# Kernel optimization log

Measured on AMD Instinct MI355X. Metric: run time of the kernel, lower is better.

## Reference

```python
import jax, jax.numpy as jnp
import numpy as np

N, D, H, G = 262144, 256, 8, 2048
DH = D // H  # 32


def setup_inputs() -> dict:
    key = jax.random.key(0)
    ks = jax.random.split(key, 12)
    s = 0.02
    x = jax.random.normal(ks[0], (N, D), jnp.float32)
    # equal-size sets: batch[i] = set id, ptr = CSR boundaries (consistent pair)
    batch = jnp.repeat(jnp.arange(G, dtype=jnp.int64), N // G)
    ptr = jnp.arange(G + 1, dtype=jnp.int64) * (N // G)
    rn = lambda k, sh: jax.random.normal(k, sh, jnp.float32) * s
    return {
        "x": x, "ptr": ptr, "batch": batch,
        "lin_w": rn(ks[1], (D, D)), "lin_b": jnp.zeros((D,), jnp.float32),
        "seed": rn(ks[2], (D,)),
        "wq": rn(ks[3], (D, D)), "bq": jnp.zeros((D,), jnp.float32),
        "wk": rn(ks[4], (D, D)), "bk": jnp.zeros((D,), jnp.float32),
        "wv": rn(ks[5], (D, D)), "bv": jnp.zeros((D,), jnp.float32),
        "wo": rn(ks[6], (D, D)), "bo": jnp.zeros((D,), jnp.float32),
        "mlp_w1": rn(ks[7], (D, D)), "mlp_b1": jnp.zeros((D,), jnp.float32),
        "mlp_w2": rn(ks[8], (D, D)), "mlp_b2": jnp.zeros((D,), jnp.float32),
    }


def gelu(v):
    return jax.nn.gelu(v, approximate=False)  # torch nn.GELU default (erf)


def reference(x, ptr, batch, lin_w, lin_b, seed, wq, bq, wk, bk, wv, bv,
              wo, bo, mlp_w1, mlp_b1, mlp_w2, mlp_b2):
    # pre-projection + GELU
    h = gelu(x @ lin_w + lin_b)                         # [N, D]
    # PMA-style multihead attention pooling over ragged sets
    q = (seed @ wq + bq).reshape(H, DH)                 # learnable seed query per head
    k = (h @ wk + bk).reshape(-1, H, DH)                # [N, H, DH]
    v = (h @ wv + bv).reshape(-1, H, DH)                # [N, H, DH]
    scores = jnp.einsum('nhd,hd->nh', k, q) / jnp.sqrt(jnp.float32(DH))  # [N, H]
    # segment (per-set) numerically-stable softmax
    m = jax.ops.segment_max(scores, batch, num_segments=G)   # [G, H]
    e = jnp.exp(scores - m[batch])
    z = jax.ops.segment_sum(e, batch, num_segments=G)        # [G, H]
    w = e / z[batch]                                         # [N, H] attention weights
    pooled = jax.ops.segment_sum(w[:, :, None] * v, batch, num_segments=G)  # [G, H, DH]
    pooled = pooled.reshape(G, D) @ wo + bo                  # output projection [G, D]
    # 2-layer MLP head (plain_last: no act on final layer; dropout=0 at eval)
    out = gelu(pooled @ mlp_w1 + mlp_b1) @ mlp_w2 + mlp_b2   # [G, D]
    return out
```

## Files before the change

### kernel.cpp

```cpp
#include <hip/hip_runtime.h>
#include <hip/hip_bf16.h>

#define DD 256
#define SETSZ 128
#define NSETS 2048

typedef __attribute__((ext_vector_type(8))) __bf16 bf16x8;
typedef __attribute__((ext_vector_type(8))) unsigned short u16x8;
typedef __attribute__((ext_vector_type(4))) float f32x4;

static __device__ __forceinline__ unsigned short f2bf(float f) {
    unsigned u = __builtin_bit_cast(unsigned, f);
    u += 0x7fffu + ((u >> 16) & 1u);
    return (unsigned short)(u >> 16);
}

static __device__ __forceinline__ float gelu_f(float v) {
    float ax = fabsf(v) * 0.70710678118654752f;
    float t = __builtin_amdgcn_rcpf(__builtin_fmaf(0.3275911f, ax, 1.0f));
    float p = __builtin_fmaf(1.061405429f, t, -1.453152027f);
    p = __builtin_fmaf(p, t, 1.421413741f);
    p = __builtin_fmaf(p, t, -0.284496736f);
    p = __builtin_fmaf(p, t, 0.254829592f);
    p = p * t;
    float er = __builtin_fmaf(-p, __expf(-ax * ax), 1.0f);
    er = copysignf(er, v);
    return 0.5f * v * (1.0f + er);
}

static __device__ __forceinline__ int swz(int row, int cg) {
    return cg ^ (row & 7) ^ ((row >> 3) & 3);
}

#define LGKM_BARRIER() do { \
    asm volatile("s_waitcnt lgkmcnt(0)" ::: "memory"); \
    __builtin_amdgcn_s_barrier(); \
} while (0)

__global__ void prep1_kernel(const float* __restrict__ seed, const float* __restrict__ wq,
                             const float* __restrict__ bq, float* __restrict__ q) {
    int j = threadIdx.x;
    float s = bq[j];
#pragma unroll 16
    for (int d = 0; d < DD; ++d) s += seed[d] * wq[d * DD + j];
    q[j] = s;
}

__global__ void prep2_kernel(const float* __restrict__ lin_w, const float* __restrict__ wv,
                             const float* __restrict__ wk, const float* __restrict__ q,
                             unsigned short* __restrict__ linT, unsigned short* __restrict__ wvT,
                             unsigned short* __restrict__ wkqB) {
    int b = blockIdx.x, t = threadIdx.x;
    if (b < DD) {
        linT[b * DD + t] = f2bf(lin_w[t * DD + b]);
        wvT[b * DD + t]  = f2bf(wv[t * DD + b]);
    } else {
        const float inv = 0.17677669529663687f;
        for (int c = 0; c < 8; ++c) {
            float s = 0.f;
#pragma unroll 8
            for (int j = 0; j < 32; ++j) s += wk[t * DD + c * 32 + j] * q[c * 32 + j];
            wkqB[c * DD + t] = f2bf(s * inv);
        }
        for (int c = 8; c < 16; ++c) wkqB[c * DD + t] = 0;
    }
}

__global__ __launch_bounds__(512, 4)
void attn_pool_kernel(const float* __restrict__ x, const float* __restrict__ lin_b,
                      const float* __restrict__ bv,
                      const unsigned short* __restrict__ linT,
                      const unsigned short* __restrict__ wvT,
                      const unsigned short* __restrict__ wkqB,
                      float* __restrict__ pooled) {
    __shared__ unsigned short xs[SETSZ * DD];
    __shared__ float wbuf[SETSZ][8];
    __shared__ float mzbuf[2][16];
    __shared__ float zbuf[2][16];
    __shared__ float pbuf[2][DD];

    const int g = blockIdx.x;
    const int t = threadIdx.x;
    const int lane = t & 63;
    const int wid = t >> 6;
    const int rh = wid >> 2;
    const int cq = wid & 3;
    const int l15 = lane & 15;
    const int kg = lane >> 4;
    const int colq = cq * 64;
    const int rowbase = rh * 64;
    const long r0 = (long)g * SETSZ;

    {
        const float* bx = x + r0 * DD;
#pragma unroll
        for (int half = 0; half < 2; ++half) {
            float4 L[8];
#pragma unroll
            for (int qq = 0; qq < 4; ++qq) {
                int c = (half * 4 + qq) * 512 + t;
                const float4* src = reinterpret_cast<const float4*>(bx + (c >> 5) * DD + (c & 31) * 8);
                L[2 * qq] = src[0];
                L[2 * qq + 1] = src[1];
            }
#pragma unroll
            for (int qq = 0; qq < 4; ++qq) {
                int c = (half * 4 + qq) * 512 + t;
                int row = c >> 5, cg = c & 31;
                u16x8 v;
                v[0] = f2bf(L[2*qq].x);   v[1] = f2bf(L[2*qq].y);
                v[2] = f2bf(L[2*qq].z);   v[3] = f2bf(L[2*qq].w);
                v[4] = f2bf(L[2*qq+1].x); v[5] = f2bf(L[2*qq+1].y);
                v[6] = f2bf(L[2*qq+1].z); v[7] = f2bf(L[2*qq+1].w);
                *reinterpret_cast<u16x8*>(&xs[row * DD + swz(row, cg) * 8]) = v;
            }
        }
    }
    LGKM_BARRIER();

    f32x4 acc[4][4];
#pragma unroll
    for (int ab = 0; ab < 4; ++ab)
#pragma unroll
        for (int nb = 0; nb < 4; ++nb) acc[ab][nb] = 0.f;

#pragma unroll
    for (int ks = 0; ks < 8; ++ks) {
        bf16x8 A[4], B[4];
#pragma unroll
        for (int ab = 0; ab < 4; ++ab)
            A[ab] = *reinterpret_cast<const bf16x8*>(linT + (colq + 16 * ab + l15) * DD + ks * 32 + kg * 8);
#pragma unroll
        for (int nb = 0; nb < 4; ++nb) {
            int row = rowbase + 16 * nb + l15;
            B[nb] = *reinterpret_cast<const bf16x8*>(&xs[row * DD + swz(row, ks * 4 + kg) * 8]);
        }
#pragma unroll
        for (int ab = 0; ab < 4; ++ab)
#pragma unroll
            for (int nb = 0; nb < 4; ++nb)
                acc[ab][nb] = __builtin_amdgcn_mfma_f32_16x16x32_bf16(A[ab], B[nb], acc[ab][nb], 0, 0, 0);
    }
    LGKM_BARRIER();

    {
#pragma unroll
        for (int ab = 0; ab < 4; ++ab) {
            const float4 lb4 = *reinterpret_cast<const float4*>(lin_b + colq + 16 * ab + 4 * kg);
            int cg = (colq >> 3) + 2 * ab + (kg >> 1);
#pragma unroll
            for (int nb = 0; nb < 4; ++nb) {
                int row = rowbase + 16 * nb + l15;
                float g0 = gelu_f(acc[ab][nb][0] + lb4.x);
                float g1 = gelu_f(acc[ab][nb][1] + lb4.y);
                float g2 = gelu_f(acc[ab][nb][2] + lb4.z);
                float g3 = gelu_f(acc[ab][nb][3] + lb4.w);
                unsigned d0 = (unsigned)f2bf(g0) | ((unsigned)f2bf(g1) << 16);
                unsigned d1 = (unsigned)f2bf(g2) | ((unsigned)f2bf(g3) << 16);
                *reinterpret_cast<uint2*>(&xs[row * DD + swz(row, cg) * 8 + (kg & 1) * 4]) =
                    make_uint2(d0, d1);
            }
        }
    }
    LGKM_BARRIER();

    f32x4 sacc[4];
    sacc[0] = 0.f; sacc[1] = 0.f; sacc[2] = 0.f; sacc[3] = 0.f;
    if (cq == 0) {
#pragma unroll
        for (int ks = 0; ks < 8; ++ks) {
            bf16x8 Aq = *reinterpret_cast<const bf16x8*>(wkqB + l15 * DD + ks * 32 + kg * 8);
#pragma unroll
            for (int nb = 0; nb < 4; ++nb) {
                int row = rowbase + 16 * nb + l15;
                bf16x8 B = *reinterpret_cast<const bf16x8*>(&xs[row * DD + swz(row, ks * 4 + kg) * 8]);
                sacc[nb] = __builtin_amdgcn_mfma_f32_16x16x32_bf16(Aq, B, sacc[nb], 0, 0, 0);
            }
        }
        float mj[4];
#pragma unroll
        for (int j = 0; j < 4; ++j)
            mj[j] = fmaxf(fmaxf(sacc[0][j], sacc[1][j]), fmaxf(sacc[2][j], sacc[3][j]));
#pragma unroll
        for (int st = 1; st < 16; st <<= 1)
#pragma unroll
            for (int j = 0; j < 4; ++j) mj[j] = fmaxf(mj[j], __shfl_xor(mj[j], st, 64));
        if (l15 == 0) {
            f32x4 mv; mv[0] = mj[0]; mv[1] = mj[1]; mv[2] = mj[2]; mv[3] = mj[3];
            *reinterpret_cast<f32x4*>(&mzbuf[rh][4 * kg]) = mv;
        }
    }
    LGKM_BARRIER();

    if (cq == 0) {
        f32x4 m0 = *reinterpret_cast<const f32x4*>(&mzbuf[0][4 * kg]);
        f32x4 m1 = *reinterpret_cast<const f32x4*>(&mzbuf[1][4 * kg]);
        float mf[4], zj[4];
#pragma unroll
        for (int j = 0; j < 4; ++j) { mf[j] = fmaxf(m0[j], m1[j]); zj[j] = 0.f; }
        f32x4 e4[4];
#pragma unroll
        for (int nb = 0; nb < 4; ++nb)
#pragma unroll
            for (int j = 0; j < 4; ++j) {
                float e = __expf(sacc[nb][j] - mf[j]);
                e4[nb][j] = e;
                zj[j] += e;
            }
#pragma unroll
        for (int st = 1; st < 16; st <<= 1)
#pragma unroll
            for (int j = 0; j < 4; ++j) zj[j] += __shfl_xor(zj[j], st, 64);
        if (l15 == 0) {
            f32x4 zv; zv[0] = zj[0]; zv[1] = zj[1]; zv[2] = zj[2]; zv[3] = zj[3];
            *reinterpret_cast<f32x4*>(&zbuf[rh][4 * kg]) = zv;
        }
        if (kg < 2) {
#pragma unroll
            for (int nb = 0; nb < 4; ++nb) {
                int row = rowbase + 16 * nb + l15;
                *reinterpret_cast<f32x4*>(&wbuf[row][4 * kg]) = e4[nb];
            }
        }
    }
    LGKM_BARRIER();

    f32x4 vacc[4][4];
#pragma unroll
    for (int ab = 0; ab < 4; ++ab)
#pragma unroll
        for (int nb = 0; nb < 4; ++nb) vacc[ab][nb] = 0.f;
#pragma unroll
    for (int ks = 0; ks < 8; ++ks) {
        bf16x8 A[4], B[4];
#pragma unroll
        for (int ab = 0; ab < 4; ++ab)
            A[ab] = *reinterpret_cast<const bf16x8*>(wvT + (colq + 16 * ab + l15) * DD + ks * 32 + kg * 8);
#pragma unroll
        for (int nb = 0; nb < 4; ++nb) {
            int row = rowbase + 16 * nb + l15;
            B[nb] = *reinterpret_cast<const bf16x8*>(&xs[row * DD + swz(row, ks * 4 + kg) * 8]);
        }
#pragma unroll
        for (int ab = 0; ab < 4; ++ab)
#pragma unroll
            for (int nb = 0; nb < 4; ++nb)
                vacc[ab][nb] = __builtin_amdgcn_mfma_f32_16x16x32_bf16(A[ab], B[nb], vacc[ab][nb], 0, 0, 0);
    }

    {
        float w0[4], w1[4];
#pragma unroll
        for (int nb = 0; nb < 4; ++nb) {
            int row = rowbase + 16 * nb + l15;
            w0[nb] = wbuf[row][2 * cq];
            w1[nb] = wbuf[row][2 * cq + 1];
        }
        float v16[16];
#pragma unroll
        for (int ab = 0; ab < 4; ++ab)
#pragma unroll
            for (int j = 0; j < 4; ++j) {
                float s = 0.f;
#pragma unroll
                for (int nb = 0; nb < 4; ++nb)
                    s += (ab < 2 ? w0[nb] : w1[nb]) * vacc[ab][nb][j];
                v16[ab * 4 + j] = s;
            }
        float v8[8], v4[4], v2[2], vf;
        {
            bool b = (l15 & 1);
#pragma unroll
            for (int i = 0; i < 8; ++i) {
                float keep = b ? v16[2 * i + 1] : v16[2 * i];
                float send = b ? v16[2 * i] : v16[2 * i + 1];
                v8[i] = keep + __shfl_xor(send, 1, 64);
            }
        }
        {
            bool b = (l15 >> 1) & 1;
#pragma unroll
            for (int i = 0; i < 4; ++i) {
                float keep = b ? v8[2 * i + 1] : v8[2 * i];
                float send = b ? v8[2 * i] : v8[2 * i + 1];
                v4[i] = keep + __shfl_xor(send, 2, 64);
            }
        }
        {
            bool b = (l15 >> 2) & 1;
#pragma unroll
            for (int i = 0; i < 2; ++i) {
                float keep = b ? v4[2 * i + 1] : v4[2 * i];
                float send = b ? v4[2 * i] : v4[2 * i + 1];
                v2[i] = keep + __shfl_xor(send, 4, 64);
            }
        }
        {
            bool b = (l15 >> 3) & 1;
            float keep = b ? v2[1] : v2[0];
            float send = b ? v2[0] : v2[1];
            vf = keep + __shfl_xor(send, 8, 64);
        }
        int vcol = colq + 16 * (l15 >> 2) + 4 * kg + (l15 & 3);
        pbuf[rh][vcol] = vf;
    }
    LGKM_BARRIER();

    if (t < DD) {
        int hh = t >> 5;
        float z = zbuf[0][hh] + zbuf[1][hh];
        pooled[(long)g * DD + t] = (pbuf[0][t] + pbuf[1][t]) / z + bv[t];
    }
}

__global__ __launch_bounds__(256)
void mlp_kernel(const float* __restrict__ pooled,
                const float* __restrict__ wo, const float* __restrict__ bo,
                const float* __restrict__ w1, const float* __restrict__ b1,
                const float* __restrict__ w2, const float* __restrict__ b2,
                float* __restrict__ out) {
    __shared__ float sa[8][DD];
    __shared__ float sb[8][DD];
    const int c = threadIdx.x;
    const long base = (long)blockIdx.x * 8 * DD;
#pragma unroll
    for (int r = 0; r < 8; ++r) sa[r][c] = pooled[base + r * DD + c];
    __syncthreads();
    {
        float acc[8];
        float bb = bo[c];
#pragma unroll
        for (int r = 0; r < 8; ++r) acc[r] = bb;
#pragma unroll 4
        for (int k = 0; k < DD; ++k) {
            float wvv = wo[k * DD + c];
#pragma unroll
            for (int r = 0; r < 8; ++r) acc[r] += sa[r][k] * wvv;
        }
#pragma unroll
        for (int r = 0; r < 8; ++r) sb[r][c] = acc[r];
    }
    __syncthreads();
    {
        float acc[8];
        float bb = b1[c];
#pragma unroll
        for (int r = 0; r < 8; ++r) acc[r] = bb;
#pragma unroll 4
        for (int k = 0; k < DD; ++k) {
            float wvv = w1[k * DD + c];
#pragma unroll
            for (int r = 0; r < 8; ++r) acc[r] += sb[r][k] * wvv;
        }
#pragma unroll
        for (int r = 0; r < 8; ++r) sa[r][c] = gelu_f(acc[r]);
    }
    __syncthreads();
    {
        float acc[8];
        float bb = b2[c];
#pragma unroll
        for (int r = 0; r < 8; ++r) acc[r] = bb;
#pragma unroll 4
        for (int k = 0; k < DD; ++k) {
            float wvv = w2[k * DD + c];
#pragma unroll
            for (int r = 0; r < 8; ++r) acc[r] += sa[r][k] * wvv;
        }
#pragma unroll
        for (int r = 0; r < 8; ++r) out[base + r * DD + c] = acc[r];
    }
}

extern "C" void kernel_launch(void* const* d_in, const int* in_sizes, int n_in,
                              void* d_out, int out_size, void* d_ws, size_t ws_size,
                              hipStream_t stream) {
    const float* x     = (const float*)d_in[0];
    const float* lin_w = (const float*)d_in[3];
    const float* lin_b = (const float*)d_in[4];
    const float* seed  = (const float*)d_in[5];
    const float* wq    = (const float*)d_in[6];
    const float* bq    = (const float*)d_in[7];
    const float* wk    = (const float*)d_in[8];
    const float* wvp   = (const float*)d_in[10];
    const float* bv    = (const float*)d_in[11];
    const float* wo    = (const float*)d_in[12];
    const float* bo    = (const float*)d_in[13];
    const float* w1    = (const float*)d_in[14];
    const float* b1    = (const float*)d_in[15];
    const float* w2    = (const float*)d_in[16];
    const float* b2    = (const float*)d_in[17];
    float* out = (float*)d_out;

    char* ws = (char*)d_ws;
    float* q             = (float*)ws;
    unsigned short* wkqB = (unsigned short*)(ws + 4096);
    unsigned short* linT = (unsigned short*)(ws + 16384);
    unsigned short* wvT  = (unsigned short*)(ws + 16384 + 131072);
    float* pooled        = (float*)(ws + 16384 + 262144);

    prep1_kernel<<<1, 256, 0, stream>>>(seed, wq, bq, q);
    prep2_kernel<<<257, 256, 0, stream>>>(lin_w, wvp, wk, q, linT, wvT, wkqB);
    attn_pool_kernel<<<NSETS, 512, 0, stream>>>(x, lin_b, bv, linT, wvT, wkqB, pooled);
    mlp_kernel<<<NSETS / 8, 256, 0, stream>>>(pooled, wo, bo, w1, b1, w2, b2, out);
}
```

Baseline: 311.1 us.

## Make attention-pool kernel persistent with double-buffered prefetch of next set

The attention-pool kernel now launches 256 persistent blocks, each looping over 8 sets. It prefetches the next set's fp32 rows into registers while the current set is computed, then converts them into a second LDS buffer. This is meant to hide global load latency behind MFMA work. The cost is double LDS use (128KB), which caps occupancy at one block per CU and raises register pressure from the 16 prefetched float4s. The weight transpose is also rewritten as a 64x64 LDS tiled transpose, and the MLP kernel now handles 4 rows per block instead of 8, giving it more blocks.

```diff
diff --git a/kernel.cpp b/kernel.cpp
--- a/kernel.cpp
+++ b/kernel.cpp
@@ -4,6 +4,8 @@
 #define DD 256
 #define SETSZ 128
 #define NSETS 2048
+#define NBLK 256
+#define SPB (NSETS / NBLK)
 
 typedef __attribute__((ext_vector_type(8))) __bf16 bf16x8;
 typedef __attribute__((ext_vector_type(8))) unsigned short u16x8;
@@ -46,14 +48,31 @@
     q[j] = s;
 }
 
-__global__ void prep2_kernel(const float* __restrict__ lin_w, const float* __restrict__ wv,
-                             const float* __restrict__ wk, const float* __restrict__ q,
-                             unsigned short* __restrict__ linT, unsigned short* __restrict__ wvT,
-                             unsigned short* __restrict__ wkqB) {
+__global__ __launch_bounds__(256)
+void prep2_kernel(const float* __restrict__ lin_w, const float* __restrict__ wv,
+                  const float* __restrict__ wk, const float* __restrict__ q,
+                  unsigned short* __restrict__ linT, unsigned short* __restrict__ wvT,
+                  unsigned short* __restrict__ wkqB) {
+    __shared__ unsigned short tl[64][65];
     int b = blockIdx.x, t = threadIdx.x;
-    if (b < DD) {
-        linT[b * DD + t] = f2bf(lin_w[t * DD + b]);
-        wvT[b * DD + t]  = f2bf(wv[t * DD + b]);
+    if (b < 32) {
+        const float* src = (b & 1) ? wv : lin_w;
+        unsigned short* dst = (b & 1) ? wvT : linT;
+        int tile = b >> 1;
+        int r0 = (tile >> 2) * 64, c0 = (tile & 3) * 64;
+#pragma unroll
+        for (int i = 0; i < 16; ++i) {
+            int idx = i * 256 + t;
+            int r = idx >> 6, c = idx & 63;
+            tl[r][c] = f2bf(src[(r0 + r) * DD + c0 + c]);
+        }
+        __syncthreads();
+#pragma unroll
+        for (int i = 0; i < 16; ++i) {
+            int idx = i * 256 + t;
+            int cc = idx >> 6, rr = idx & 63;
+            dst[(c0 + cc) * DD + r0 + rr] = tl[rr][cc];
+        }
     } else {
         const float inv = 0.17677669529663687f;
         for (int c = 0; c < 8; ++c) {
@@ -66,20 +85,19 @@
     }
 }
 
-__global__ __launch_bounds__(512, 4)
+__global__ __launch_bounds__(512, 1)
 void attn_pool_kernel(const float* __restrict__ x, const float* __restrict__ lin_b,
                       const float* __restrict__ bv,
                       const unsigned short* __restrict__ linT,
                       const unsigned short* __restrict__ wvT,
                       const unsigned short* __restrict__ wkqB,
                       float* __restrict__ pooled) {
-    __shared__ unsigned short xs[SETSZ * DD];
+    __shared__ unsigned short bufs[2][SETSZ * DD];
     __shared__ float wbuf[SETSZ][8];
     __shared__ float mzbuf[2][16];
     __shared__ float zbuf[2][16];
     __shared__ float pbuf[2][DD];
 
-    const int g = blockIdx.x;
     const int t = threadIdx.x;
     const int lane = t & 63;
     const int wid = t >> 6;
@@ -89,61 +107,68 @@
     const int kg = lane >> 4;
     const int colq = cq * 64;
     const int rowbase = rh * 64;
-    const long r0 = (long)g * SETSZ;
+    const long set0 = (long)blockIdx.x * SPB;
 
     {
-        const float* bx = x + r0 * DD;
-#pragma unroll
-        for (int half = 0; half < 2; ++half) {
-            float4 L[8];
-#pragma unroll
-            for (int qq = 0; qq < 4; ++qq) {
-                int c = (half * 4 + qq) * 512 + t;
-                const float4* src = reinterpret_cast<const float4*>(bx + (c >> 5) * DD + (c & 31) * 8);
-                L[2 * qq] = src[0];
-                L[2 * qq + 1] = src[1];
-            }
-#pragma unroll
-            for (int qq = 0; qq < 4; ++qq) {
-                int c = (half * 4 + qq) * 512 + t;
-                int row = c >> 5, cg = c & 31;
-                u16x8 v;
-                v[0] = f2bf(L[2*qq].x);   v[1] = f2bf(L[2*qq].y);
-                v[2] = f2bf(L[2*qq].z);   v[3] = f2bf(L[2*qq].w);
-                v[4] = f2bf(L[2*qq+1].x); v[5] = f2bf(L[2*qq+1].y);
-                v[6] = f2bf(L[2*qq+1].z); v[7] = f2bf(L[2*qq+1].w);
-                *reinterpret_cast<u16x8*>(&xs[row * DD + swz(row, cg) * 8]) = v;
-            }
+        const float* nb = x + set0 * SETSZ * DD;
+#pragma unroll
+        for (int i = 0; i < 8; ++i) {
+            int p = i * 512 + t;
+            float4 a = *reinterpret_cast<const float4*>(nb + p * 8);
+            float4 b = *reinterpret_cast<const float4*>(nb + p * 8 + 4);
+            int row = p >> 5, cg = p & 31;
+            u16x8 v;
+            v[0] = f2bf(a.x); v[1] = f2bf(a.y); v[2] = f2bf(a.z); v[3] = f2bf(a.w);
+            v[4] = f2bf(b.x); v[5] = f2bf(b.y); v[6] = f2bf(b.z); v[7] = f2bf(b.w);
+            *reinterpret_cast<u16x8*>(&bufs[0][row * DD + swz(row, cg) * 8]) = v;
         }
     }
     LGKM_BARRIER();
 
-    f32x4 acc[4][4];
-#pragma unroll
-    for (int ab = 0; ab < 4; ++ab)
-#pragma unroll
-        for (int nb = 0; nb < 4; ++nb) acc[ab][nb] = 0.f;
-
-#pragma unroll
-    for (int ks = 0; ks < 8; ++ks) {
-        bf16x8 A[4], B[4];
+    int cur = 0;
+    for (int s = 0; s < SPB; ++s) {
+        const unsigned short* xs = bufs[cur];
+        unsigned short* xsm = bufs[cur];
+        unsigned short* xn = bufs[cur ^ 1];
+        const bool pf_on = (s + 1 < SPB);
+
+        float4 pf[16];
+        if (pf_on) {
+            const float* nb = x + (set0 + s + 1) * SETSZ * DD;
+#pragma unroll
+            for (int i = 0; i < 8; ++i) {
+                int p = i * 512 + t;
+                pf[2 * i]     = *reinterpret_cast<const float4*>(nb + p * 8);
+                pf[2 * i + 1] = *reinterpret_cast<const float4*>(nb + p * 8 + 4);
+            }
+        }
+        __builtin_amdgcn_sched_barrier(0);
+
+        f32x4 acc[4][4];
 #pragma unroll
         for (int ab = 0; ab < 4; ++ab)
-            A[ab] = *reinterpret_cast<const bf16x8*>(linT + (colq + 16 * ab + l15) * DD + ks * 32 + kg * 8);
-#pragma unroll
-        for (int nb = 0; nb < 4; ++nb) {
-            int row = rowbase + 16 * nb + l15;
-            B[nb] = *reinterpret_cast<const bf16x8*>(&xs[row * DD + swz(row, ks * 4 + kg) * 8]);
-        }
-#pragma unroll
-        for (int ab = 0; ab < 4; ++ab)
-#pragma unroll
-            for (int nb = 0; nb < 4; ++nb)
-                acc[ab][nb] = __builtin_amdgcn_mfma_f32_16x16x32_bf16(A[ab], B[nb], acc[ab][nb], 0, 0, 0);
-    }
-    LGKM_BARRIER();
-
-    {
+#pragma unroll
+            for (int nb = 0; nb < 4; ++nb) acc[ab][nb] = 0.f;
+
+#pragma unroll
+        for (int ks = 0; ks < 8; ++ks) {
+            bf16x8 A[4], B[4];
+#pragma unroll
+            for (int ab = 0; ab < 4; ++ab)
+                A[ab] = *reinterpret_cast<const bf16x8*>(linT + (colq + 16 * ab + l15) * DD + ks * 32 + kg * 8);
+#pragma unroll
+            for (int nb = 0; nb < 4; ++nb) {
+                int row = rowbase + 16 * nb + l15;
+                B[nb] = *reinterpret_cast<const bf16x8*>(&xs[row * DD + swz(row, ks * 4 + kg) * 8]);
+            }
+#pragma unroll
+            for (int ab = 0; ab < 4; ++ab)
+#pragma unroll
+                for (int nb = 0; nb < 4; ++nb)
+                    acc[ab][nb] = __builtin_amdgcn_mfma_f32_16x16x32_bf16(A[ab], B[nb], acc[ab][nb], 0, 0, 0);
+        }
+        LGKM_BARRIER();
+
 #pragma unroll
         for (int ab = 0; ab < 4; ++ab) {
             const float4 lb4 = *reinterpret_cast<const float4*>(lin_b + colq + 16 * ab + 4 * kg);
@@ -157,159 +182,174 @@
                 float g3 = gelu_f(acc[ab][nb][3] + lb4.w);
                 unsigned d0 = (unsigned)f2bf(g0) | ((unsigned)f2bf(g1) << 16);
                 unsigned d1 = (unsigned)f2bf(g2) | ((unsigned)f2bf(g3) << 16);
-                *reinterpret_cast<uint2*>(&xs[row * DD + swz(row, cg) * 8 + (kg & 1) * 4]) =
+                *reinterpret_cast<uint2*>(&xsm[row * DD + swz(row, cg) * 8 + (kg & 1) * 4]) =
                     make_uint2(d0, d1);
             }
         }
-    }
-    LGKM_BARRIER();
-
-    f32x4 sacc[4];
-    sacc[0] = 0.f; sacc[1] = 0.f; sacc[2] = 0.f; sacc[3] = 0.f;
-    if (cq == 0) {
+        LGKM_BARRIER();
+
+        f32x4 sacc[4];
+        sacc[0] = 0.f; sacc[1] = 0.f; sacc[2] = 0.f; sacc[3] = 0.f;
+        if (cq == 0) {
+#pragma unroll
+            for (int ks = 0; ks < 8; ++ks) {
+                bf16x8 Aq = *reinterpret_cast<const bf16x8*>(wkqB + l15 * DD + ks * 32 + kg * 8);
+#pragma unroll
+                for (int nb = 0; nb < 4; ++nb) {
+                    int row = rowbase + 16 * nb + l15;
+                    bf16x8 B = *reinterpret_cast<const bf16x8*>(&xs[row * DD + swz(row, ks * 4 + kg) * 8]);
+                    sacc[nb] = __builtin_amdgcn_mfma_f32_16x16x32_bf16(Aq, B, sacc[nb], 0, 0, 0);
+                }
+            }
+            float mj[4];
+#pragma unroll
+            for (int j = 0; j < 4; ++j)
+                mj[j] = fmaxf(fmaxf(sacc[0][j], sacc[1][j]), fmaxf(sacc[2][j], sacc[3][j]));
+#pragma unroll
+            for (int st = 1; st < 16; st <<= 1)
+#pragma unroll
+                for (int j = 0; j < 4; ++j) mj[j] = fmaxf(mj[j], __shfl_xor(mj[j], st, 64));
+            if (l15 == 0) {
+                f32x4 mv; mv[0] = mj[0]; mv[1] = mj[1]; mv[2] = mj[2]; mv[3] = mj[3];
+                *reinterpret_cast<f32x4*>(&mzbuf[rh][4 * kg]) = mv;
+            }
+        }
+        LGKM_BARRIER();
+
+        if (cq == 0) {
+            f32x4 m0 = *reinterpret_cast<const f32x4*>(&mzbuf[0][4 * kg]);
+            f32x4 m1 = *reinterpret_cast<const f32x4*>(&mzbuf[1][4 * kg]);
+            float mf[4], zj[4];
+#pragma unroll
+            for (int j = 0; j < 4; ++j) { mf[j] = fmaxf(m0[j], m1[j]); zj[j] = 0.f; }
+            f32x4 e4[4];
+#pragma unroll
+            for (int nb = 0; nb < 4; ++nb)
+#pragma unroll
+                for (int j = 0; j < 4; ++j) {
+                    float e = __expf(sacc[nb][j] - mf[j]);
+                    e4[nb][j] = e;
+                    zj[j] += e;
+                }
+#pragma unroll
+            for (int st = 1; st < 16; st <<= 1)
+#pragma unroll
+                for (int j = 0; j < 4; ++j) zj[j] += __shfl_xor(zj[j], st, 64);
+            if (l15 == 0) {
+                f32x4 zv; zv[0] = zj[0]; zv[1] = zj[1]; zv[2] = zj[2]; zv[3] = zj[3];
+                *reinterpret_cast<f32x4*>(&zbuf[rh][4 * kg]) = zv;
+            }
+            if (kg < 2) {
+#pragma unroll
+                for (int nb = 0; nb < 4; ++nb) {
+                    int row = rowbase + 16 * nb + l15;
+                    *reinterpret_cast<f32x4*>(&wbuf[row][4 * kg]) = e4[nb];
+                }
+            }
+        }
+        LGKM_BARRIER();
+
+        f32x4 vacc[4][4];
+#pragma unroll
+        for (int ab = 0; ab < 4; ++ab)
+#pragma unroll
+            for (int nb = 0; nb < 4; ++nb) vacc[ab][nb] = 0.f;
 #pragma unroll
         for (int ks = 0; ks < 8; ++ks) {
-            bf16x8 Aq = *reinterpret_cast<const bf16x8*>(wkqB + l15 * DD + ks * 32 + kg * 8);
+            bf16x8 A[4], B[4];
+#pragma unroll
+            for (int ab = 0; ab < 4; ++ab)
+                A[ab] = *reinterpret_cast<const bf16x8*>(wvT + (colq + 16 * ab + l15) * DD + ks * 32 + kg * 8);
 #pragma unroll
             for (int nb = 0; nb < 4; ++nb) {
                 int row = rowbase + 16 * nb + l15;
-                bf16x8 B = *reinterpret_cast<const bf16x8*>(&xs[row * DD + swz(row, ks * 4 + kg) * 8]);
-                sacc[nb] = __builtin_amdgcn_mfma_f32_16x16x32_bf16(Aq, B, sacc[nb], 0, 0, 0);
-            }
-        }
-        float mj[4];
-#pragma unroll
-        for (int j = 0; j < 4; ++j)
-            mj[j] = fmaxf(fmaxf(sacc[0][j], sacc[1][j]), fmaxf(sacc[2][j], sacc[3][j]));
-#pragma unroll
-        for (int st = 1; st < 16; st <<= 1)
-#pragma unroll
-            for (int j = 0; j < 4; ++j) mj[j] = fmaxf(mj[j], __shfl_xor(mj[j], st, 64));
-        if (l15 == 0) {
-            f32x4 mv; mv[0] = mj[0]; mv[1] = mj[1]; mv[2] = mj[2]; mv[3] = mj[3];
-            *reinterpret_cast<f32x4*>(&mzbuf[rh][4 * kg]) = mv;
-        }
-    }
-    LGKM_BARRIER();
-
-    if (cq == 0) {
-        f32x4 m0 = *reinterpret_cast<const f32x4*>(&mzbuf[0][4 * kg]);
-        f32x4 m1 = *reinterpret_cast<const f32x4*>(&mzbuf[1][4 * kg]);
-        float mf[4], zj[4];
-#pragma unroll
-        for (int j = 0; j < 4; ++j) { mf[j] = fmaxf(m0[j], m1[j]); zj[j] = 0.f; }
-        f32x4 e4[4];
-#pragma unroll
-        for (int nb = 0; nb < 4; ++nb)
-#pragma unroll
-            for (int j = 0; j < 4; ++j) {
-                float e = __expf(sacc[nb][j] - mf[j]);
-                e4[nb][j] = e;
-                zj[j] += e;
-            }
-#pragma unroll
-        for (int st = 1; st < 16; st <<= 1)
-#pragma unroll
-            for (int j = 0; j < 4; ++j) zj[j] += __shfl_xor(zj[j], st, 64);
-        if (l15 == 0) {
-            f32x4 zv; zv[0] = zj[0]; zv[1] = zj[1]; zv[2] = zj[2]; zv[3] = zj[3];
-            *reinterpret_cast<f32x4*>(&zbuf[rh][4 * kg]) = zv;
-        }
-        if (kg < 2) {
+                B[nb] = *reinterpret_cast<const bf16x8*>(&xs[row * DD + swz(row, ks * 4 + kg) * 8]);
+            }
+#pragma unroll
+            for (int ab = 0; ab < 4; ++ab)
+#pragma unroll
+                for (int nb = 0; nb < 4; ++nb)
+                    vacc[ab][nb] = __builtin_amdgcn_mfma_f32_16x16x32_bf16(A[ab], B[nb], vacc[ab][nb], 0, 0, 0);
+        }
+
+        {
+            float w0[4], w1[4];
 #pragma unroll
             for (int nb = 0; nb < 4; ++nb) {
                 int row = rowbase + 16 * nb + l15;
-                *reinterpret_cast<f32x4*>(&wbuf[row][4 * kg]) = e4[nb];
-            }
-        }
-    }
-    LGKM_BARRIER();
-
-    f32x4 vacc[4][4];
-#pragma unroll
-    for (int ab = 0; ab < 4; ++ab)
-#pragma unroll
-        for (int nb = 0; nb < 4; ++nb) vacc[ab][nb] = 0.f;
-#pragma unroll
-    for (int ks = 0; ks < 8; ++ks) {
-        bf16x8 A[4], B[4];
-#pragma unroll
-        for (int ab = 0; ab < 4; ++ab)
-            A[ab] = *reinterpret_cast<const bf16x8*>(wvT + (colq + 16 * ab + l15) * DD + ks * 32 + kg * 8);
-#pragma unroll
-        for (int nb = 0; nb < 4; ++nb) {
-            int row = rowbase + 16 * nb + l15;
-            B[nb] = *reinterpret_cast<const bf16x8*>(&xs[row * DD + swz(row, ks * 4 + kg) * 8]);
-        }
-#pragma unroll
-        for (int ab = 0; ab < 4; ++ab)
-#pragma unroll
-            for (int nb = 0; nb < 4; ++nb)
-                vacc[ab][nb] = __builtin_amdgcn_mfma_f32_16x16x32_bf16(A[ab], B[nb], vacc[ab][nb], 0, 0, 0);
-    }
-
-    {
-        float w0[4], w1[4];
-#pragma unroll
-        for (int nb = 0; nb < 4; ++nb) {
-            int row = rowbase + 16 * nb + l15;
-            w0[nb] = wbuf[row][2 * cq];
-            w1[nb] = wbuf[row][2 * cq + 1];
-        }
-        float v16[16];
-#pragma unroll
-        for (int ab = 0; ab < 4; ++ab)
-#pragma unroll
-            for (int j = 0; j < 4; ++j) {
-                float s = 0.f;
-#pragma unroll
-                for (int nb = 0; nb < 4; ++nb)
-                    s += (ab < 2 ? w0[nb] : w1[nb]) * vacc[ab][nb][j];
-                v16[ab * 4 + j] = s;
-            }
-        float v8[8], v4[4], v2[2], vf;
-        {
-            bool b = (l15 & 1);
+                w0[nb] = wbuf[row][2 * cq];
+                w1[nb] = wbuf[row][2 * cq + 1];
+            }
+            float v16[16];
+#pragma unroll
+            for (int ab = 0; ab < 4; ++ab)
+#pragma unroll
+                for (int j = 0; j < 4; ++j) {
+                    float sum = 0.f;
+#pragma unroll
+                    for (int nb = 0; nb < 4; ++nb)
+                        sum += (ab < 2 ? w0[nb] : w1[nb]) * vacc[ab][nb][j];
+                    v16[ab * 4 + j] = sum;
+                }
+            float v8[8], v4[4], v2[2], vf;
+            {
+                bool bb = (l15 & 1);
+#pragma unroll
+                for (int i = 0; i < 8; ++i) {
+                    float keep = bb ? v16[2 * i + 1] : v16[2 * i];
+                    float send = bb ? v16[2 * i] : v16[2 * i + 1];
+                    v8[i] = keep + __shfl_xor(send, 1, 64);
+                }
+            }
+            {
+                bool bb = (l15 >> 1) & 1;
+#pragma unroll
+                for (int i = 0; i < 4; ++i) {
+                    float keep = bb ? v8[2 * i + 1] : v8[2 * i];
+                    float send = bb ? v8[2 * i] : v8[2 * i + 1];
+                    v4[i] = keep + __shfl_xor(send, 2, 64);
+                }
+            }
+            {
+                bool bb = (l15 >> 2) & 1;
+#pragma unroll
+                for (int i = 0; i < 2; ++i) {
+                    float keep = bb ? v4[2 * i + 1] : v4[2 * i];
+                    float send = bb ? v4[2 * i] : v4[2 * i + 1];
+                    v2[i] = keep + __shfl_xor(send, 4, 64);
+                }
+            }
+            {
+                bool bb = (l15 >> 3) & 1;
+                float keep = bb ? v2[1] : v2[0];
+                float send = bb ? v2[0] : v2[1];
+                vf = keep + __shfl_xor(send, 8, 64);
+            }
+            int vcol = colq + 16 * (l15 >> 2) + 4 * kg + (l15 & 3);
+            pbuf[rh][vcol] = vf;
+        }
+        LGKM_BARRIER();
+
+        if (t < DD) {
+            int hh = t >> 5;
+            float zz = zbuf[0][hh] + zbuf[1][hh];
+            pooled[(set0 + s) * DD + t] = (pbuf[0][t] + pbuf[1][t]) / zz + bv[t];
+        }
+        if (pf_on) {
 #pragma unroll
             for (int i = 0; i < 8; ++i) {
-                float keep = b ? v16[2 * i + 1] : v16[2 * i];
-                float send = b ? v16[2 * i] : v16[2 * i + 1];
-                v8[i] = keep + __shfl_xor(send, 1, 64);
-            }
-        }
-        {
-            bool b = (l15 >> 1) & 1;
-#pragma unroll
-            for (int i = 0; i < 4; ++i) {
-                float keep = b ? v8[2 * i + 1] : v8[2 * i];
-                float send = b ? v8[2 * i] : v8[2 * i + 1];
-                v4[i] = keep + __shfl_xor(send, 2, 64);
-            }
-        }
-        {
-            bool b = (l15 >> 2) & 1;
-#pragma unroll
-            for (int i = 0; i < 2; ++i) {
-                float keep = b ? v4[2 * i + 1] : v4[2 * i];
-                float send = b ? v4[2 * i] : v4[2 * i + 1];
-                v2[i] = keep + __shfl_xor(send, 4, 64);
-            }
-        }
-        {
-            bool b = (l15 >> 3) & 1;
-            float keep = b ? v2[1] : v2[0];
-            float send = b ? v2[0] : v2[1];
-            vf = keep + __shfl_xor(send, 8, 64);
-        }
-        int vcol = colq + 16 * (l15 >> 2) + 4 * kg + (l15 & 3);
-        pbuf[rh][vcol] = vf;
-    }
-    LGKM_BARRIER();
-
-    if (t < DD) {
-        int hh = t >> 5;
-        float z = zbuf[0][hh] + zbuf[1][hh];
-        pooled[(long)g * DD + t] = (pbuf[0][t] + pbuf[1][t]) / z + bv[t];
+                int p = i * 512 + t;
+                int row = p >> 5, cg = p & 31;
+                u16x8 v;
+                v[0] = f2bf(pf[2*i].x);   v[1] = f2bf(pf[2*i].y);
+                v[2] = f2bf(pf[2*i].z);   v[3] = f2bf(pf[2*i].w);
+                v[4] = f2bf(pf[2*i+1].x); v[5] = f2bf(pf[2*i+1].y);
+                v[6] = f2bf(pf[2*i+1].z); v[7] = f2bf(pf[2*i+1].w);
+                *reinterpret_cast<u16x8*>(&xn[row * DD + swz(row, cg) * 8]) = v;
+            }
+        }
+        LGKM_BARRIER();
+        cur ^= 1;
     }
 }
 
@@ -319,56 +359,56 @@
                 const float* __restrict__ w1, const float* __restrict__ b1,
                 const float* __restrict__ w2, const float* __restrict__ b2,
                 float* __restrict__ out) {
-    __shared__ float sa[8][DD];
-    __shared__ float sb[8][DD];
+    __shared__ float sa[4][DD];
+    __shared__ float sb[4][DD];
     const int c = threadIdx.x;
-    const long base = (long)blockIdx.x * 8 * DD;
-#pragma unroll
-    for (int r = 0; r < 8; ++r) sa[r][c] = pooled[base + r * DD + c];
+    const long base = (long)blockIdx.x * 4 * DD;
+#pragma unroll
+    for (int r = 0; r < 4; ++r) sa[r][c] = pooled[base + r * DD + c];
     __syncthreads();
     {
-        float acc[8];
+        float acc[4];
         float bb = bo[c];
 #pragma unroll
-        for (int r = 0; r < 8; ++r) acc[r] = bb;
-#pragma unroll 4
+        for (int r = 0; r < 4; ++r) acc[r] = bb;
+#pragma unroll 8
         for (int k = 0; k < DD; ++k) {
             float wvv = wo[k * DD + c];
 #pragma unroll
-            for (int r = 0; r < 8; ++r) acc[r] += sa[r][k] * wvv;
-        }
-#pragma unroll
-        for (int r = 0; r < 8; ++r) sb[r][c] = acc[r];
+            for (int r = 0; r < 4; ++r) acc[r] += sa[r][k] * wvv;
+        }
+#pragma unroll
+        for (int r = 0; r < 4; ++r) sb[r][c] = acc[r];
     }
     __syncthreads();
     {
-        float acc[8];
+        float acc[4];
         float bb = b1[c];
 #pragma unroll
-        for (int r = 0; r < 8; ++r) acc[r] = bb;
-#pragma unroll 4
+        for (int r = 0; r < 4; ++r) acc[r] = bb;
+#pragma unroll 8
         for (int k = 0; k < DD; ++k) {
             float wvv = w1[k * DD + c];
 #pragma unroll
-            for (int r = 0; r < 8; ++r) acc[r] += sb[r][k] * wvv;
-        }
-#pragma unroll
-        for (int r = 0; r < 8; ++r) sa[r][c] = gelu_f(acc[r]);
+            for (int r = 0; r < 4; ++r) acc[r] += sb[r][k] * wvv;
+        }
+#pragma unroll
+        for (int r = 0; r < 4; ++r) sa[r][c] = gelu_f(acc[r]);
     }
     __syncthreads();
     {
-        float acc[8];
+        float acc[4];
         float bb = b2[c];
 #pragma unroll
-        for (int r = 0; r < 8; ++r) acc[r] = bb;
-#pragma unroll 4
+        for (int r = 0; r < 4; ++r) acc[r] = bb;
+#pragma unroll 8
         for (int k = 0; k < DD; ++k) {
             float wvv = w2[k * DD + c];
 #pragma unroll
-            for (int r = 0; r < 8; ++r) acc[r] += sa[r][k] * wvv;
-        }
-#pragma unroll
-        for (int r = 0; r < 8; ++r) out[base + r * DD + c] = acc[r];
+            for (int r = 0; r < 4; ++r) acc[r] += sa[r][k] * wvv;
+        }
+#pragma unroll
+        for (int r = 0; r < 4; ++r) out[base + r * DD + c] = acc[r];
     }
 }
 
@@ -400,7 +440,7 @@
     float* pooled        = (float*)(ws + 16384 + 262144);
 
     prep1_kernel<<<1, 256, 0, stream>>>(seed, wq, bq, q);
-    prep2_kernel<<<257, 256, 0, stream>>>(lin_w, wvp, wk, q, linT, wvT, wkqB);
-    attn_pool_kernel<<<NSETS, 512, 0, stream>>>(x, lin_b, bv, linT, wvT, wkqB, pooled);
-    mlp_kernel<<<NSETS / 8, 256, 0, stream>>>(pooled, wo, bo, w1, b1, w2, b2, out);
-}
+    prep2_kernel<<<33, 256, 0, stream>>>(lin_w, wvp, wk, q, linT, wvT, wkqB);
+    attn_pool_kernel<<<NBLK, 512, 0, stream>>>(x, lin_b, bv, linT, wvT, wkqB, pooled);
+    mlp_kernel<<<NSETS / 4, 256, 0, stream>>>(pooled, wo, bo, w1, b1, w2, b2, out);
+}
```

Result: slower. 415.3 us (+33.5%).
